# Performance work log

Measured on AMD Instinct MI355X. Metric: run time of the kernel, lower is better.

The kernel has to match this reference:

```python
import jax, jax.numpy as jnp
import numpy as np

NEG_SLOPE = 0.2


def gat_layer(x_src, x_dst, src, dst, W, a_src, a_dst, b, n_dst, H, C):
    # Linear transform: [Ns, H, C] / [Nd, H, C]
    h_s = (x_src @ W).reshape(-1, H, C)
    h_d = (x_dst @ W).reshape(-1, H, C)
    # Per-edge attention logits: a . [x_i || x_j] (x_i = dst/target, x_j = src)
    e = jnp.einsum('ehc,hc->eh', h_s[src], a_src) + jnp.einsum('ehc,hc->eh', h_d[dst], a_dst)
    e = jax.nn.leaky_relu(e, NEG_SLOPE)  # [E, H]
    # Segment softmax over destination neighborhoods
    m = jax.ops.segment_max(e, dst, num_segments=n_dst)          # [Nd, H]
    ex = jnp.exp(e - m[dst])
    denom = jax.ops.segment_sum(ex, dst, num_segments=n_dst)    # [Nd, H]
    alpha = ex / denom[dst]                                      # [E, H]
    # Weighted scatter-sum aggregation
    out = jax.ops.segment_sum(alpha[:, :, None] * h_s[src], dst, num_segments=n_dst)
    return out.reshape(n_dst, H * C) + b


def setup_inputs() -> dict:
    key = jax.random.key(0)
    ks = jax.random.split(key, 16)
    N, F_IN, OUT = 200000, 602, 41
    N1, N1D, E1 = 120000, 30000, 960000
    N2D, E2 = 6000, 192000
    s = 0.05
    return {
        'x': jax.random.normal(ks[0], (N, F_IN), jnp.float32),
        'n_id1': jax.random.randint(ks[1], (N1,), 0, N),
        'res_n_id1': jax.random.randint(ks[2], (N1D,), 0, N1),
        'edge_src1': jax.random.randint(ks[3], (E1,), 0, N1),
        'edge_dst1': jax.random.randint(ks[4], (E1,), 0, N1D),
        'res_n_id2': jax.random.randint(ks[5], (N2D,), 0, N1D),
        'edge_src2': jax.random.randint(ks[6], (E2,), 0, N1D),
        'edge_dst2': jax.random.randint(ks[7], (E2,), 0, N2D),
        'W1': jax.random.normal(ks[8], (F_IN, 64), jnp.float32) * s,
        'att_src1': jax.random.normal(ks[9], (8, 8), jnp.float32) * s,
        'att_dst1': jax.random.normal(ks[10], (8, 8), jnp.float32) * s,
        'bias1': jax.random.normal(ks[11], (64,), jnp.float32) * s,
        'W2': jax.random.normal(ks[12], (64, OUT), jnp.float32) * s,
        'att_src2': jax.random.normal(ks[13], (1, OUT), jnp.float32) * s,
        'att_dst2': jax.random.normal(ks[14], (1, OUT), jnp.float32) * s,
        'bias2': jax.random.normal(ks[15], (OUT,), jnp.float32) * s,
    }


def reference(x, n_id1, res_n_id1, edge_src1, edge_dst1, res_n_id2, edge_src2,
              edge_dst2, W1, att_src1, att_dst1, bias1, W2, att_src2, att_dst2, bias2):
    # Block 1: gather frontier, GATConv(in -> 8, heads=8, concat) -> [N1D, 64]
    h = x[n_id1]
    h = gat_layer(h, h[res_n_id1], edge_src1, edge_dst1,
                  W1, att_src1, att_dst1, bias1, res_n_id1.shape[0], 8, 8)
    h = jax.nn.elu(h)
    # (dropout p=0.6 is identity in eval mode)
    # Block 2: GATConv(64 -> out, heads=1) -> [N2D, out]
    h = gat_layer(h, h[res_n_id2], edge_src2, edge_dst2,
                  W2, att_src2, att_dst2, bias2, res_n_id2.shape[0], 1, W2.shape[1])
    return jax.nn.log_softmax(h, axis=1)
```

## Files before the change

kernel.cpp:

```cpp
#include <hip/hip_runtime.h>
#include <hip/hip_bf16.h>
#include <math.h>

typedef __attribute__((ext_vector_type(8))) short short8;
typedef __attribute__((ext_vector_type(4))) float float4v;
typedef unsigned short ushort_t;

__device__ __forceinline__ float wave_max64(float v) {
#pragma unroll
  for (int o = 32; o > 0; o >>= 1) v = fmaxf(v, __shfl_xor(v, o));
  return v;
}
__device__ __forceinline__ float wave_sum64(float v) {
#pragma unroll
  for (int o = 32; o > 0; o >>= 1) v += __shfl_xor(v, o);
  return v;
}
__device__ __forceinline__ int wave_isum64(int v) {
#pragma unroll
  for (int o = 32; o > 0; o >>= 1) v += __shfl_xor(v, o);
  return v;
}
__device__ __forceinline__ float lrelu02(float v) { return v > 0.f ? v : 0.2f * v; }
__device__ __forceinline__ short bf16_rne(float f) {
  unsigned u = __builtin_bit_cast(unsigned, f);
  unsigned r = (u + 0x7FFFu + ((u >> 16) & 1u)) >> 16;
  return (short)r;
}
__device__ __forceinline__ float bf16_to_f32(ushort_t u) {
  return __builtin_bit_cast(float, ((unsigned)u) << 16);
}

__global__ void hist_prepack_kernel(const int* __restrict__ dst1, const int* __restrict__ dst2,
                                    int* __restrict__ counts, int* __restrict__ erank,
                                    const float* __restrict__ W,
                                    short* __restrict__ Wp, int E1, int E2, int N1D, int nbE) {
  int b = blockIdx.x;
  if (b < nbE) {
    int e = b * 256 + threadIdx.x;
    if (e < E1) {
      erank[e] = atomicAdd(&counts[dst1[e]], 1);
    } else if (e < E1 + E2) {
      erank[e] = atomicAdd(&counts[N1D + dst2[e - E1]], 1);
    }
  } else {
    int idx = (b - nbE) * 256 + threadIdx.x;
    if (idx >= 19 * 4 * 64) return;
    int lane = idx & 63;
    int t = (idx >> 6) & 3;
    int s = idx >> 8;
    int quad = lane >> 4, n = t * 16 + (lane & 15);
    short8 v;
#pragma unroll
    for (int j = 0; j < 8; j++) {
      int k = s * 32 + quad * 8 + j;
      v[j] = (k < 602) ? bf16_rne(W[k * 64 + n]) : (short)0;
    }
    *((short8*)Wp + idx) = v;
  }
}

__global__ __launch_bounds__(256) void scan1_kernel(const int* __restrict__ counts,
                                                    int* __restrict__ offs,
                                                    int* __restrict__ bsum, int n) {
  __shared__ int ws[4], wpre[4];
  int tid = threadIdx.x, lane = tid & 63, w = tid >> 6;
  int i = blockIdx.x * 256 + tid;
  int v = (i < n) ? counts[i] : 0;
  int x = v;
#pragma unroll
  for (int o = 1; o < 64; o <<= 1) {
    int y = __shfl_up(x, o);
    if (lane >= o) x += y;
  }
  if (lane == 63) ws[w] = x;
  __syncthreads();
  if (tid == 0) {
    int run = 0;
#pragma unroll
    for (int k = 0; k < 4; k++) { wpre[k] = run; run += ws[k]; }
    bsum[blockIdx.x] = run;
  }
  __syncthreads();
  if (i < n) offs[i] = x - v + wpre[w];
}

__global__ __launch_bounds__(256) void scan3_kernel(int* __restrict__ offs,
                                                    const int* __restrict__ bsum,
                                                    int n, int etot, int nb) {
  __shared__ int wsum[4];
  int tid = threadIdx.x, lane = tid & 63, w = tid >> 6;
  int bid = blockIdx.x;
  int v = (tid < nb && tid < bid) ? bsum[tid] : 0;
  v = wave_isum64(v);
  if (lane == 0) wsum[w] = v;
  __syncthreads();
  int pre = wsum[0] + wsum[1] + wsum[2] + wsum[3];
  int i = bid * 256 + tid;
  if (i < n) offs[i] += pre;
  if (i == 0) offs[n] = etot;
}

__global__ __launch_bounds__(256) void gemm1_fused_kernel(
    const float* __restrict__ x, const int* __restrict__ n_id,
    const short* __restrict__ Wp, const float* __restrict__ as1,
    ushort_t* __restrict__ out, float* __restrict__ ssrc1, int M, int nbE,
    const int* __restrict__ dst1, const int* __restrict__ src1,
    const int* __restrict__ dst2, const int* __restrict__ src2,
    const int* __restrict__ offs, const int* __restrict__ erank,
    int* __restrict__ epay, int E1, int E2, int N1D) {
  if (blockIdx.x < nbE) {
    int e = blockIdx.x * 256 + threadIdx.x;
    if (e < E1) {
      int d = dst1[e];
      epay[offs[d] + erank[e]] = src1[e];
    } else if (e < E1 + E2) {
      int e2 = e - E1;
      int d = N1D + dst2[e2];
      epay[offs[d] + erank[e]] = src2[e2];
    }
    return;
  }
  constexpr int K = 602, NSTEP = 19;
  int gb = blockIdx.x - nbE;
  int tid = threadIdx.x;
  int wid = tid >> 6, lane = tid & 63;
  int quad = lane >> 4, mrow = lane & 15;
  int r = gb * 64 + wid * 16 + mrow;
  int grow = n_id[r < M ? r : M - 1];
  const float* xrow = x + (size_t)grow * K;
  float4v acc[4] = {{0.f, 0.f, 0.f, 0.f}, {0.f, 0.f, 0.f, 0.f},
                    {0.f, 0.f, 0.f, 0.f}, {0.f, 0.f, 0.f, 0.f}};
  for (int s = 0; s < NSTEP; s++) {
    int k0 = s * 32 + quad * 8;
    float af[8];
    if (k0 + 8 <= K) {
#pragma unroll
      for (int j = 0; j < 8; j += 2) {
        float2 v = *(const float2*)(xrow + k0 + j);
        af[j] = v.x;
        af[j + 1] = v.y;
      }
    } else {
#pragma unroll
      for (int j = 0; j < 8; j++) af[j] = (k0 + j < K) ? xrow[k0 + j] : 0.f;
    }
    short8 a;
#pragma unroll
    for (int j = 0; j < 8; j++) a[j] = bf16_rne(af[j]);
    const short8* wp = (const short8*)Wp + (size_t)s * 256 + lane;
#pragma unroll
    for (int t = 0; t < 4; t++) {
      short8 b = wp[t * 64];
      acc[t] = __builtin_amdgcn_mfma_f32_16x16x32_bf16(a, b, acc[t], 0, 0, 0);
    }
  }
  int rb = gb * 64 + wid * 16;
#pragma unroll
  for (int t = 0; t < 4; t++) {
#pragma unroll
    for (int j = 0; j < 4; j++) {
      int rr = rb + quad * 4 + j;
      if (rr < M) out[(size_t)rr * 64 + t * 16 + mrow] = (ushort_t)bf16_rne(acc[t][j]);
    }
  }
  float afv[4];
#pragma unroll
  for (int t = 0; t < 4; t++) afv[t] = as1[t * 16 + mrow];
#pragma unroll
  for (int t = 0; t < 4; t++) {
#pragma unroll
    for (int j = 0; j < 4; j++) {
      float v = acc[t][j] * afv[t];
      v += __shfl_xor(v, 1);
      v += __shfl_xor(v, 2);
      v += __shfl_xor(v, 4);
      if ((lane & 7) == 0) {
        int rr = rb + quad * 4 + j;
        if (rr < M) ssrc1[rr * 8 + t * 2 + ((lane >> 3) & 1)] = v;
      }
    }
  }
}

__global__ __launch_bounds__(256) void agg1_kernel(
    const int* __restrict__ offs, const int* __restrict__ srcs,
    const float* __restrict__ s_src, const int* __restrict__ res,
    const float* __restrict__ ad, const ushort_t* __restrict__ hs1,
    const float* __restrict__ bias, const float* __restrict__ W2,
    const float* __restrict__ as2, float* __restrict__ hs2,
    float* __restrict__ ssrc2, int n_dst) {
  constexpr int C = 41;
  __shared__ float Ws[64 * C];
  __shared__ float rowsh[4][64];
  for (int i = threadIdx.x; i < 64 * C; i += 256) Ws[i] = W2[i];
  __syncthreads();
  int wid = (blockIdx.x * blockDim.x + threadIdx.x) >> 6;
  if (wid >= n_dst) return;
  int lane = threadIdx.x & 63;
  int w = threadIdx.x >> 6;
  int h = lane >> 3;
  int node = res[wid];
  float v = bf16_to_f32(hs1[(size_t)node * 64 + lane]) * ad[lane];
  v += __shfl_xor(v, 1);
  v += __shfl_xor(v, 2);
  v += __shfl_xor(v, 4);
  float sd = v;
  int beg = offs[wid], end = offs[wid + 1];
  float mx = -1e30f, den = 0.f, acc = 0.f;
  for (int i = beg; i < end; i += 8) {
    int m = end - i; if (m > 8) m = 8;
    int sr[8]; float ss[8], row[8];
#pragma unroll
    for (int j = 0; j < 8; j++) sr[j] = srcs[i + (j < m ? j : 0)];
#pragma unroll
    for (int j = 0; j < 8; j++) ss[j] = s_src[sr[j] * 8 + h];
#pragma unroll
    for (int j = 0; j < 8; j++) row[j] = bf16_to_f32(hs1[(size_t)sr[j] * 64 + lane]);
    float p[8];
#pragma unroll
    for (int j = 0; j < 8; j++) p[j] = (j < m) ? lrelu02(ss[j] + sd) : -1e30f;
    float bm = mx;
#pragma unroll
    for (int j = 0; j < 8; j++) bm = fmaxf(bm, p[j]);
    float scale = __expf(mx - bm);
    den *= scale;
    acc *= scale;
#pragma unroll
    for (int j = 0; j < 8; j++) {
      float w2 = __expf(p[j] - bm);
      den += w2;
      acc += w2 * row[j];
    }
    mx = bm;
  }
  float val = (end > beg) ? acc / den : 0.f;
  val += bias[lane];
  val = val > 0.f ? val : __expf(val) - 1.f;
  rowsh[w][lane] = val;
  float acc2 = 0.f;
  if (lane < C) {
#pragma unroll 8
    for (int k = 0; k < 64; k++) acc2 += rowsh[w][k] * Ws[k * C + lane];
  }
  float tt = (lane < C) ? acc2 * as2[lane] : 0.f;
  tt = wave_sum64(tt);
  if (lane == 0) ssrc2[wid] = tt;
  if (lane < C) hs2[(size_t)wid * C + lane] = acc2;
}

__global__ __launch_bounds__(256) void agg2_kernel(
    const int* __restrict__ offs, const int* __restrict__ srcs,
    const float* __restrict__ s_src, const int* __restrict__ res,
    const float* __restrict__ ad, const float* __restrict__ hs2,
    const float* __restrict__ bias, float* __restrict__ out, int n_dst) {
  constexpr int C = 41;
  int wid = (blockIdx.x * blockDim.x + threadIdx.x) >> 6;
  if (wid >= n_dst) return;
  int lane = threadIdx.x & 63;
  bool act = lane < C;
  int node = res[wid];
  float dv = act ? hs2[(size_t)node * C + lane] * ad[lane] : 0.f;
  float sd = wave_sum64(dv);
  int beg = offs[wid], end = offs[wid + 1];
  float mx = -1e30f, den = 0.f, acc = 0.f;
  for (int i = beg; i < end; i += 8) {
    int m = end - i; if (m > 8) m = 8;
    int sr[8]; float ss[8], row[8];
#pragma unroll
    for (int j = 0; j < 8; j++) sr[j] = srcs[i + (j < m ? j : 0)];
#pragma unroll
    for (int j = 0; j < 8; j++) ss[j] = s_src[sr[j]];
#pragma unroll
    for (int j = 0; j < 8; j++) row[j] = act ? hs2[(size_t)sr[j] * C + lane] : 0.f;
    float p[8];
#pragma unroll
    for (int j = 0; j < 8; j++) p[j] = (j < m) ? lrelu02(ss[j] + sd) : -1e30f;
    float bm = mx;
#pragma unroll
    for (int j = 0; j < 8; j++) bm = fmaxf(bm, p[j]);
    float scale = __expf(mx - bm);
    den *= scale;
    acc *= scale;
#pragma unroll
    for (int j = 0; j < 8; j++) {
      float w = __expf(p[j] - bm);
      den += w;
      acc += w * row[j];
    }
    mx = bm;
  }
  float val = (end > beg) ? acc / den : 0.f;
  if (act) val += bias[lane];
  float lv = act ? val : -1e30f;
  float m2 = wave_max64(lv);
  float ex = act ? __expf(val - m2) : 0.f;
  float ssum = wave_sum64(ex);
  if (act) out[(size_t)wid * C + lane] = val - m2 - __logf(ssum);
}

extern "C" void kernel_launch(void* const* d_in, const int* in_sizes, int n_in,
                              void* d_out, int out_size, void* d_ws, size_t ws_size,
                              hipStream_t stream) {
  const float* x    = (const float*)d_in[0];
  const int* n_id1  = (const int*)d_in[1];
  const int* res1   = (const int*)d_in[2];
  const int* esrc1  = (const int*)d_in[3];
  const int* edst1  = (const int*)d_in[4];
  const int* res2   = (const int*)d_in[5];
  const int* esrc2  = (const int*)d_in[6];
  const int* edst2  = (const int*)d_in[7];
  const float* W1   = (const float*)d_in[8];
  const float* as1  = (const float*)d_in[9];
  const float* ad1  = (const float*)d_in[10];
  const float* b1   = (const float*)d_in[11];
  const float* W2   = (const float*)d_in[12];
  const float* as2  = (const float*)d_in[13];
  const float* ad2  = (const float*)d_in[14];
  const float* b2   = (const float*)d_in[15];
  float* out = (float*)d_out;

  const int N1  = in_sizes[1];
  const int N1D = in_sizes[2];
  const int E1  = in_sizes[3];
  const int N2D = in_sizes[5];
  const int E2  = in_sizes[6];
  const int NTOT = N1D + N2D;
  const int ETOT = E1 + E2;

  char* w = (char*)d_ws;
  size_t off = 0;
  auto alloc = [&](size_t bytes) -> void* {
    void* p = (void*)(w + off);
    off += (bytes + 255) & ~(size_t)255;
    return p;
  };
  ushort_t* hs1 = (ushort_t*)alloc((size_t)N1 * 64 * 2);
  float* ssrc1 = (float*)alloc((size_t)N1 * 8 * 4);
  float* hs2   = (float*)alloc((size_t)N1D * 41 * 4);
  float* ssrc2 = (float*)alloc((size_t)N1D * 4);
  int* counts  = (int*)alloc((size_t)NTOT * 4);
  int* offs    = (int*)alloc((size_t)(NTOT + 1) * 4);
  int* bsum    = (int*)alloc((size_t)256 * 4);
  int* epay    = (int*)alloc((size_t)ETOT * 4);
  int* erank   = (int*)alloc((size_t)ETOT * 4);
  short* Wp    = (short*)alloc((size_t)19 * 4 * 64 * 8 * 2);
  (void)ws_size; (void)n_in; (void)out_size;

  hipMemsetAsync(counts, 0, (size_t)NTOT * 4, stream);

  const int nbE = (ETOT + 255) / 256;
  const int nb = (NTOT + 255) / 256;
  hist_prepack_kernel<<<nbE + 19, 256, 0, stream>>>(edst1, edst2, counts, erank, W1, Wp,
                                                    E1, E2, N1D, nbE);
  scan1_kernel<<<nb, 256, 0, stream>>>(counts, offs, bsum, NTOT);
  scan3_kernel<<<nb, 256, 0, stream>>>(offs, bsum, NTOT, ETOT, nb);

  const int nbG = (N1 + 63) / 64;
  gemm1_fused_kernel<<<nbE + nbG, 256, 0, stream>>>(
      x, n_id1, Wp, as1, hs1, ssrc1, N1, nbE,
      edst1, esrc1, edst2, esrc2, offs, erank, epay, E1, E2, N1D);
  agg1_kernel<<<(N1D + 3) / 4, 256, 0, stream>>>(offs, epay, ssrc1, res1, ad1, hs1, b1,
                                                 W2, as2, hs2, ssrc2, N1D);

  agg2_kernel<<<(N2D + 3) / 4, 256, 0, stream>>>(offs + N1D, epay, ssrc2, res2, ad2, hs2, b2, out, N2D);
}
```

Before: 785.4 us.

## Merge scan kernels via grid barrier, vectorize edge passes, prefetch GEMM A rows

The two-kernel prefix scan becomes a single kernel. Each block publishes its partial sum and spins on a global done counter until every block has arrived, then computes its own prefix. The histogram and edge-scatter passes now process four edges per thread with int4 loads, and the GEMM loop prefetches the next K-step of x into registers to overlap load latency with MFMA. The spin barrier assumes all 118 scan blocks are co-resident, which holds on this GPU but is not formally guaranteed.

```diff
diff --git a/kernel.cpp b/kernel.cpp
--- a/kernel.cpp
+++ b/kernel.cpp
@@ -34,17 +34,38 @@
 __global__ void hist_prepack_kernel(const int* __restrict__ dst1, const int* __restrict__ dst2,
                                     int* __restrict__ counts, int* __restrict__ erank,
                                     const float* __restrict__ W,
-                                    short* __restrict__ Wp, int E1, int E2, int N1D, int nbE) {
+                                    short* __restrict__ Wp, int E1, int E2, int N1D, int nbE4) {
   int b = blockIdx.x;
-  if (b < nbE) {
-    int e = b * 256 + threadIdx.x;
-    if (e < E1) {
-      erank[e] = atomicAdd(&counts[dst1[e]], 1);
-    } else if (e < E1 + E2) {
-      erank[e] = atomicAdd(&counts[N1D + dst2[e - E1]], 1);
+  if (b < nbE4) {
+    int base = (b * 256 + threadIdx.x) * 4;
+    if (base + 3 < E1) {
+      int4 d = *(const int4*)(dst1 + base);
+      int4 r;
+      r.x = atomicAdd(&counts[d.x], 1);
+      r.y = atomicAdd(&counts[d.y], 1);
+      r.z = atomicAdd(&counts[d.z], 1);
+      r.w = atomicAdd(&counts[d.w], 1);
+      *(int4*)(erank + base) = r;
+    } else if (base < E1) {
+      for (int j = 0; j < 4 && base + j < E1; j++)
+        erank[base + j] = atomicAdd(&counts[dst1[base + j]], 1);
+    } else {
+      int base2 = base - E1;
+      if (base2 + 3 < E2) {
+        int4 d = *(const int4*)(dst2 + base2);
+        int4 r;
+        r.x = atomicAdd(&counts[N1D + d.x], 1);
+        r.y = atomicAdd(&counts[N1D + d.y], 1);
+        r.z = atomicAdd(&counts[N1D + d.z], 1);
+        r.w = atomicAdd(&counts[N1D + d.w], 1);
+        *(int4*)(erank + base) = r;
+      } else {
+        for (int j = 0; j < 4 && base2 + j < E2; j++)
+          erank[base + j] = atomicAdd(&counts[N1D + dst2[base2 + j]], 1);
+      }
     }
   } else {
-    int idx = (b - nbE) * 256 + threadIdx.x;
+    int idx = (b - nbE4) * 256 + threadIdx.x;
     if (idx >= 19 * 4 * 64) return;
     int lane = idx & 63;
     int t = (idx >> 6) & 3;
@@ -60,12 +81,15 @@
   }
 }
 
-__global__ __launch_bounds__(256) void scan1_kernel(const int* __restrict__ counts,
-                                                    int* __restrict__ offs,
-                                                    int* __restrict__ bsum, int n) {
-  __shared__ int ws[4], wpre[4];
+__global__ __launch_bounds__(256) void scan_kernel(const int* __restrict__ counts,
+                                                   int* __restrict__ offs,
+                                                   int* __restrict__ bsum,
+                                                   int* __restrict__ done,
+                                                   int n, int etot, int nb) {
+  __shared__ int ws[4], wpre[4], wsum[4];
   int tid = threadIdx.x, lane = tid & 63, w = tid >> 6;
-  int i = blockIdx.x * 256 + tid;
+  int bid = blockIdx.x;
+  int i = bid * 256 + tid;
   int v = (i < n) ? counts[i] : 0;
   int x = v;
 #pragma unroll
@@ -79,50 +103,62 @@
     int run = 0;
 #pragma unroll
     for (int k = 0; k < 4; k++) { wpre[k] = run; run += ws[k]; }
-    bsum[blockIdx.x] = run;
+    __hip_atomic_store(&bsum[bid], run, __ATOMIC_RELEASE, __HIP_MEMORY_SCOPE_AGENT);
+    __hip_atomic_fetch_add(done, 1, __ATOMIC_RELEASE, __HIP_MEMORY_SCOPE_AGENT);
+    while (__hip_atomic_load(done, __ATOMIC_ACQUIRE, __HIP_MEMORY_SCOPE_AGENT) < nb) {}
   }
   __syncthreads();
-  if (i < n) offs[i] = x - v + wpre[w];
-}
-
-__global__ __launch_bounds__(256) void scan3_kernel(int* __restrict__ offs,
-                                                    const int* __restrict__ bsum,
-                                                    int n, int etot, int nb) {
-  __shared__ int wsum[4];
-  int tid = threadIdx.x, lane = tid & 63, w = tid >> 6;
-  int bid = blockIdx.x;
-  int v = (tid < nb && tid < bid) ? bsum[tid] : 0;
-  v = wave_isum64(v);
-  if (lane == 0) wsum[w] = v;
+  int pv = (tid < nb && tid < bid)
+               ? __hip_atomic_load(&bsum[tid], __ATOMIC_RELAXED, __HIP_MEMORY_SCOPE_AGENT)
+               : 0;
+  pv = wave_isum64(pv);
+  if (lane == 0) wsum[w] = pv;
   __syncthreads();
   int pre = wsum[0] + wsum[1] + wsum[2] + wsum[3];
-  int i = bid * 256 + tid;
-  if (i < n) offs[i] += pre;
+  if (i < n) offs[i] = x - v + wpre[w] + pre;
   if (i == 0) offs[n] = etot;
 }
 
 __global__ __launch_bounds__(256) void gemm1_fused_kernel(
     const float* __restrict__ x, const int* __restrict__ n_id,
     const short* __restrict__ Wp, const float* __restrict__ as1,
-    ushort_t* __restrict__ out, float* __restrict__ ssrc1, int M, int nbE,
+    ushort_t* __restrict__ out, float* __restrict__ ssrc1, int M, int nbE4,
     const int* __restrict__ dst1, const int* __restrict__ src1,
     const int* __restrict__ dst2, const int* __restrict__ src2,
     const int* __restrict__ offs, const int* __restrict__ erank,
     int* __restrict__ epay, int E1, int E2, int N1D) {
-  if (blockIdx.x < nbE) {
-    int e = blockIdx.x * 256 + threadIdx.x;
-    if (e < E1) {
-      int d = dst1[e];
-      epay[offs[d] + erank[e]] = src1[e];
-    } else if (e < E1 + E2) {
-      int e2 = e - E1;
-      int d = N1D + dst2[e2];
-      epay[offs[d] + erank[e]] = src2[e2];
+  if (blockIdx.x < nbE4) {
+    int base = (blockIdx.x * 256 + threadIdx.x) * 4;
+    if (base + 3 < E1) {
+      int4 d = *(const int4*)(dst1 + base);
+      int4 s = *(const int4*)(src1 + base);
+      int4 r = *(const int4*)(erank + base);
+      epay[offs[d.x] + r.x] = s.x;
+      epay[offs[d.y] + r.y] = s.y;
+      epay[offs[d.z] + r.z] = s.z;
+      epay[offs[d.w] + r.w] = s.w;
+    } else if (base < E1) {
+      for (int j = 0; j < 4 && base + j < E1; j++)
+        epay[offs[dst1[base + j]] + erank[base + j]] = src1[base + j];
+    } else {
+      int base2 = base - E1;
+      if (base2 + 3 < E2) {
+        int4 d = *(const int4*)(dst2 + base2);
+        int4 s = *(const int4*)(src2 + base2);
+        int4 r = *(const int4*)(erank + base);
+        epay[offs[N1D + d.x] + r.x] = s.x;
+        epay[offs[N1D + d.y] + r.y] = s.y;
+        epay[offs[N1D + d.z] + r.z] = s.z;
+        epay[offs[N1D + d.w] + r.w] = s.w;
+      } else {
+        for (int j = 0; j < 4 && base2 + j < E2; j++)
+          epay[offs[N1D + dst2[base2 + j]] + erank[base + j]] = src2[base2 + j];
+      }
     }
     return;
   }
   constexpr int K = 602, NSTEP = 19;
-  int gb = blockIdx.x - nbE;
+  int gb = blockIdx.x - nbE4;
   int tid = threadIdx.x;
   int wid = tid >> 6, lane = tid & 63;
   int quad = lane >> 4, mrow = lane & 15;
@@ -131,29 +167,40 @@
   const float* xrow = x + (size_t)grow * K;
   float4v acc[4] = {{0.f, 0.f, 0.f, 0.f}, {0.f, 0.f, 0.f, 0.f},
                     {0.f, 0.f, 0.f, 0.f}, {0.f, 0.f, 0.f, 0.f}};
+  float2 cur[4], nxt[4];
+  auto ld = [&](int s, float2* b) {
+    int k0 = s * 32 + quad * 8;
+    if (k0 + 8 <= K) {
+#pragma unroll
+      for (int j = 0; j < 4; j++) b[j] = *(const float2*)(xrow + k0 + 2 * j);
+    } else {
+#pragma unroll
+      for (int j = 0; j < 4; j++) {
+        int k = k0 + 2 * j;
+        float2 t;
+        t.x = (k < K) ? xrow[k] : 0.f;
+        t.y = (k + 1 < K) ? xrow[k + 1] : 0.f;
+        b[j] = t;
+      }
+    }
+  };
+  ld(0, cur);
   for (int s = 0; s < NSTEP; s++) {
-    int k0 = s * 32 + quad * 8;
-    float af[8];
-    if (k0 + 8 <= K) {
-#pragma unroll
-      for (int j = 0; j < 8; j += 2) {
-        float2 v = *(const float2*)(xrow + k0 + j);
-        af[j] = v.x;
-        af[j + 1] = v.y;
-      }
-    } else {
-#pragma unroll
-      for (int j = 0; j < 8; j++) af[j] = (k0 + j < K) ? xrow[k0 + j] : 0.f;
-    }
+    if (s + 1 < NSTEP) ld(s + 1, nxt);
     short8 a;
 #pragma unroll
-    for (int j = 0; j < 8; j++) a[j] = bf16_rne(af[j]);
+    for (int j = 0; j < 4; j++) {
+      a[2 * j] = bf16_rne(cur[j].x);
+      a[2 * j + 1] = bf16_rne(cur[j].y);
+    }
     const short8* wp = (const short8*)Wp + (size_t)s * 256 + lane;
 #pragma unroll
     for (int t = 0; t < 4; t++) {
-      short8 b = wp[t * 64];
-      acc[t] = __builtin_amdgcn_mfma_f32_16x16x32_bf16(a, b, acc[t], 0, 0, 0);
-    }
+      short8 bfr = wp[t * 64];
+      acc[t] = __builtin_amdgcn_mfma_f32_16x16x32_bf16(a, bfr, acc[t], 0, 0, 0);
+    }
+#pragma unroll
+    for (int j = 0; j < 4; j++) cur[j] = nxt[j];
   }
   int rb = gb * 64 + wid * 16;
 #pragma unroll
@@ -339,7 +386,8 @@
   float* ssrc1 = (float*)alloc((size_t)N1 * 8 * 4);
   float* hs2   = (float*)alloc((size_t)N1D * 41 * 4);
   float* ssrc2 = (float*)alloc((size_t)N1D * 4);
-  int* counts  = (int*)alloc((size_t)NTOT * 4);
+  int* counts  = (int*)alloc((size_t)(NTOT + 1) * 4);
+  int* done    = counts + NTOT;
   int* offs    = (int*)alloc((size_t)(NTOT + 1) * 4);
   int* bsum    = (int*)alloc((size_t)256 * 4);
   int* epay    = (int*)alloc((size_t)ETOT * 4);
@@ -347,18 +395,17 @@
   short* Wp    = (short*)alloc((size_t)19 * 4 * 64 * 8 * 2);
   (void)ws_size; (void)n_in; (void)out_size;
 
-  hipMemsetAsync(counts, 0, (size_t)NTOT * 4, stream);
-
-  const int nbE = (ETOT + 255) / 256;
+  hipMemsetAsync(counts, 0, (size_t)(NTOT + 1) * 4, stream);
+
+  const int nbE4 = (ETOT + 1023) / 1024;
   const int nb = (NTOT + 255) / 256;
-  hist_prepack_kernel<<<nbE + 19, 256, 0, stream>>>(edst1, edst2, counts, erank, W1, Wp,
-                                                    E1, E2, N1D, nbE);
-  scan1_kernel<<<nb, 256, 0, stream>>>(counts, offs, bsum, NTOT);
-  scan3_kernel<<<nb, 256, 0, stream>>>(offs, bsum, NTOT, ETOT, nb);
+  hist_prepack_kernel<<<nbE4 + 19, 256, 0, stream>>>(edst1, edst2, counts, erank, W1, Wp,
+                                                     E1, E2, N1D, nbE4);
+  scan_kernel<<<nb, 256, 0, stream>>>(counts, offs, bsum, done, NTOT, ETOT, nb);
 
   const int nbG = (N1 + 63) / 64;
-  gemm1_fused_kernel<<<nbE + nbG, 256, 0, stream>>>(
-      x, n_id1, Wp, as1, hs1, ssrc1, N1, nbE,
+  gemm1_fused_kernel<<<nbE4 + nbG, 256, 0, stream>>>(
+      x, n_id1, Wp, as1, hs1, ssrc1, N1, nbE4,
       edst1, esrc1, edst2, esrc2, offs, erank, epay, E1, E2, N1D);
   agg1_kernel<<<(N1D + 3) / 4, 256, 0, stream>>>(offs, epay, ssrc1, res1, ad1, hs1, b1,
                                                  W2, as2, hs2, ssrc2, N1D);
```

New measurement: 783.4 us. About the same (-0.3%).
